# Kernel optimization log

Measured on AMD Instinct MI355X. Metric: run time of the kernel, lower is better.

## Reference

```python
import jax, jax.numpy as jnp
import numpy as np

ITEM_NUM = 50000
EMBED = 256          # d4 = 64, d2 = 128
HIDDEN = 128
BETA = 0.5
BATCH = 4096
HIST = 50
K_NEAR = 10


def setup_inputs() -> dict:
    key = jax.random.key(0)
    ks = jax.random.split(key, 12)
    d4, d2 = EMBED // 4, EMBED // 2
    return {
        "history": jax.random.randint(ks[0], (BATCH, HIST), 0, ITEM_NUM),
        "target": jax.random.randint(ks[1], (BATCH,), 0, ITEM_NUM),
        "near_pois": jax.random.randint(ks[2], (ITEM_NUM, K_NEAR), 0, ITEM_NUM),
        "target_region": jax.random.randint(ks[3], (BATCH,), 0, 1000),
        "E_in": jax.random.normal(ks[4], (ITEM_NUM, d4), jnp.float32) * 0.01,
        "E_out": jax.random.normal(ks[5], (ITEM_NUM, d4), jnp.float32) * 0.01,
        "E_hist": jax.random.normal(ks[6], (ITEM_NUM, d2), jnp.float32) * 0.01,
        "E_targ": jax.random.normal(ks[7], (ITEM_NUM, d2), jnp.float32) * 0.01,
        "W1": jax.random.normal(ks[8], (HIDDEN, EMBED), jnp.float32) * 0.02,
        "b1": jnp.zeros((HIDDEN,), jnp.float32),
        "W2": jax.random.normal(ks[9], (1, HIDDEN), jnp.float32) * 0.02,
    }


def _self_attn(q_src, kv):
    # q = row 0 of q_src; key is a RESHAPE (not transpose) of kv, faithful to torch code.
    N, K, d = kv.shape
    q = q_src[:, 0:1, :]                      # [N,1,d]
    k = kv.reshape(N, d, K)                   # [N,d,K] (reshape, matching torch)
    scores = jnp.einsum('nod,ndk->nok', q, k) / jnp.sqrt(jnp.float32(d))
    w = jax.nn.softmax(scores, axis=-1)       # [N,1,K]
    return jnp.einsum('nok,nkd->nod', w, kv)[:, 0, :]  # [N,d]


def reference(history, target, near_pois, target_region,
              E_in, E_out, E_hist, E_targ, W1, b1, W2):
    ingoing = E_in[near_pois]                 # [N,K,d4]
    outgoing = E_out[near_pois]               # [N,K,d4]
    region_out = _self_attn(ingoing, outgoing)   # [N,d4]
    region_in = _self_attn(outgoing, ingoing)    # [N,d4]

    hist_region = jnp.concatenate([region_in[history], region_out[history]], -1)  # [B,H,d2]
    targ_region = jnp.concatenate([region_out[target], region_in[target]], -1)    # [B,d2]

    hist = jnp.concatenate([E_hist[history], hist_region], -1)      # [B,H,E]
    targ = jnp.concatenate([E_targ[target], targ_region], -1)       # [B,E]

    x = hist * targ[:, None, :]                                     # [B,H,E]
    h1 = jax.nn.relu(x @ W1.T + b1)                                 # [B,H,hidden] (dropout = eval/identity)
    scores = (h1 @ W2.T)[..., 0]                                    # [B,H]

    mask = (history != target[:, None])
    expA = jnp.exp(scores) * mask                                   # [B,H]
    denom = jnp.sum(expA, axis=-1) ** BETA                          # [B], power-normalized (non-softmax)
    w = expA / denom[:, None]                                       # [B,H]

    pred = jnp.einsum('bhe,bh,be->b', hist, w, targ)                # weighted bmm reduction
    return jax.nn.sigmoid(pred)
```

## Files before the change

### kernel.cpp

```cpp
#include <hip/hip_runtime.h>
#include <hip/hip_bf16.h>
#include <math.h>

#define EMBED 256
#define HIDDEN 128
#define NBATCH 4096
#define HISTN 50
#define KNEAR 10
#define D4 64
#define ITEMN 50000
#define XSB 272

#define SH 64.0f
#define SW 32.0f
#define INV_SXSW (1.0f / 32768.0f)
#define INV_SX (1.0f / 1024.0f)

typedef __attribute__((ext_vector_type(4))) float floatx4;
typedef __attribute__((ext_vector_type(2))) float floatx2;

__device__ inline unsigned short f2bf(float f) {
    union { __hip_bfloat16 h; unsigned short u; } cv;
    cv.h = __float2bfloat16(f);
    return cv.u;
}
__device__ inline float bf2f(unsigned short u) {
    return __uint_as_float(((unsigned)u) << 16);
}
__device__ inline unsigned pack2(float a, float b) {
    return (unsigned)f2bf(a) | ((unsigned)f2bf(b) << 16);
}
__device__ inline unsigned pk_fp8x4(float a, float b, float c, float d) {
    int v = __builtin_amdgcn_cvt_pk_fp8_f32(a, b, 0, false);
    v = __builtin_amdgcn_cvt_pk_fp8_f32(c, d, v, true);
    return (unsigned)v;
}
__device__ inline void up_fp8x4(unsigned u, float* f) {
    floatx2 lo = __builtin_amdgcn_cvt_pk_f32_fp8((int)u, false);
    floatx2 hi = __builtin_amdgcn_cvt_pk_f32_fp8((int)u, true);
    f[0] = lo.x; f[1] = lo.y; f[2] = hi.x; f[3] = hi.y;
}

template<int CTRL>
__device__ __forceinline__ float dppf(float x) {
    return __uint_as_float((unsigned)__builtin_amdgcn_update_dpp(
        0, (int)__float_as_uint(x), CTRL, 0xF, 0xF, true));
}
#define DPP_XOR1 0xB1
#define DPP_XOR2 0x4E
#define DPP_HMIR 0x141
#define DPP_MIR  0x140

__global__ __launch_bounds__(256) void fuse1(
    const int* __restrict__ np,
    const float* __restrict__ E_in, const float* __restrict__ E_out,
    const float* __restrict__ E_hist, const float* __restrict__ W1,
    unsigned char* __restrict__ histT, unsigned char* __restrict__ W1s)
{
    __shared__ unsigned short tb_all[4][20 * 64];

    if (blockIdx.x < ITEMN / 4) {
        const int wv = threadIdx.x >> 6;
        const int lane = threadIdx.x & 63;
        const int n = blockIdx.x * 4 + wv;
        unsigned short* tb = tb_all[wv];

        const int g16 = lane >> 4, c16 = lane & 15;

#pragma unroll
        for (int j = 0; j < 5; ++j) {
            int cr = 4 * j + g16;
            int rsel = (cr < 10) ? cr : cr - 10;
            int item = np[n * KNEAR + rsel];
            const float* srcf = ((cr < 10) ? E_in : E_out)
                                + (size_t)item * D4 + c16 * 4;
            float4 v = *(const float4*)srcf;
            uint2 w;
            w.x = pack2(v.x, v.y);
            w.y = pack2(v.z, v.w);
            *(uint2*)&tb[cr * 64 + c16 * 4] = w;
        }
        __asm__ volatile("s_waitcnt lgkmcnt(0)" ::: "memory");

        const int kk = c16;
        const int par = lane & 1, cp = lane >> 1;

#pragma unroll
        for (int pass = 0; pass < 2; ++pass) {
            const int qb = pass ? 640 : 0;
            const int kb = pass ? 0 : 640;

            uint4 qa = *(const uint4*)&tb[qb + g16 * 16];
            uint4 qc = *(const uint4*)&tb[qb + g16 * 16 + 8];
            float qf[16];
            {
                unsigned wds[8] = {qa.x, qa.y, qa.z, qa.w, qc.x, qc.y, qc.z, qc.w};
#pragma unroll
                for (int m = 0; m < 8; ++m) {
                    qf[2 * m]     = bf2f((unsigned short)(wds[m] & 0xffff));
                    qf[2 * m + 1] = bf2f((unsigned short)(wds[m] >> 16));
                }
            }

            const unsigned short* kvp = &tb[kb + g16 * 160 + kk];
            float p = 0.f;
#pragma unroll
            for (int i = 0; i < 16; ++i)
                p = fmaf(bf2f(kvp[10 * i]), qf[i], p);
            p += __shfl_xor(p, 16);
            p += __shfl_xor(p, 32);
            float sc = p * 0.125f;

            float mv = (kk < 10) ? sc : -1e30f;
            mv = fmaxf(mv, dppf<DPP_XOR1>(mv));
            mv = fmaxf(mv, dppf<DPP_XOR2>(mv));
            mv = fmaxf(mv, dppf<DPP_HMIR>(mv));
            mv = fmaxf(mv, dppf<DPP_MIR>(mv));
            float e = (kk < 10) ? __expf(sc - mv) : 0.f;
            float s = e;
            s += dppf<DPP_XOR1>(s);
            s += dppf<DPP_XOR2>(s);
            s += dppf<DPP_HMIR>(s);
            s += dppf<DPP_MIR>(s);
            float w = e / s;

            float oc0 = 0.f, oc1 = 0.f;
#pragma unroll
            for (int q = 0; q < 5; ++q) {
                float we = __uint_as_float(__builtin_amdgcn_readlane(__float_as_uint(w), 2 * q));
                float wo = __uint_as_float(__builtin_amdgcn_readlane(__float_as_uint(w), 2 * q + 1));
                float ws = par ? wo : we;
                unsigned v = *(const unsigned*)&tb[kb + (2 * q + par) * 64 + cp * 2];
                oc0 = fmaf(bf2f((unsigned short)(v & 0xffff)), ws, oc0);
                oc1 = fmaf(bf2f((unsigned short)(v >> 16)), ws, oc1);
            }
            oc0 += dppf<DPP_XOR1>(oc0);
            oc1 += dppf<DPP_XOR1>(oc1);
            if (!par) {
                unsigned char* dst = histT + (size_t)n * 256
                                     + (pass ? 128 : 192) + cp * 2;
                int v2 = __builtin_amdgcn_cvt_pk_fp8_f32(oc0 * SH, oc1 * SH, 0, false);
                *(unsigned short*)dst = (unsigned short)(v2 & 0xffff);
            }
        }
        return;
    }

    long t = (long)(blockIdx.x - ITEMN / 4) * 256 + threadIdx.x;
    if (t < (long)ITEMN * 16) {
        int row = (int)(t >> 4);
        int c8 = ((int)t & 15) * 8;
        const float4* s = (const float4*)&E_hist[(size_t)row * 128 + c8];
        float4 a = s[0], b = s[1];
        uint2 o;
        o.x = pk_fp8x4(a.x * SH, a.y * SH, a.z * SH, a.w * SH);
        o.y = pk_fp8x4(b.x * SH, b.y * SH, b.z * SH, b.w * SH);
        *(uint2*)&histT[(size_t)row * 256 + c8] = o;
        return;
    }
    t -= (long)ITEMN * 16;
    if (t < 4096) {
        int l = (int)t & 63;
        int f = (int)t >> 6;
        int k = f >> 3, nt = f & 7;
        int row = nt * 16 + (l & 15);
        int col = k * 32 + ((l >> 4) << 3);
        const float* src = W1 + row * EMBED + col;
        uint2 o;
        o.x = pk_fp8x4(src[0] * SW, src[1] * SW, src[2] * SW, src[3] * SW);
        o.y = pk_fp8x4(src[4] * SW, src[5] * SW, src[6] * SW, src[7] * SW);
        *(uint2*)&W1s[(size_t)t * 8] = o;
    }
}

__global__ __launch_bounds__(256, 6) void score_kernel(
    const int* __restrict__ history, const int* __restrict__ target,
    const unsigned char* __restrict__ histT,
    const float* __restrict__ E_targ,
    const unsigned char* __restrict__ W1s,
    const float* __restrict__ b1, const float* __restrict__ W2,
    float* __restrict__ out)
{
    __shared__ __align__(16) unsigned char Xs[64][XSB];
    __shared__ float scoreP[4][64];
    __shared__ float rowsumS[64];

    const int t = threadIdx.x;
    const int lane = t & 63;
    const int wv = t >> 6;
    const int b = blockIdx.x;
    const int ti = target[b];
    const int nt0 = wv * 2;
    const int c4 = lane * 4;

    float tgs[4];
    if (c4 < 128) {
        float4 v = *(const float4*)&E_targ[(size_t)ti * 128 + c4];
        tgs[0] = v.x * 16.f; tgs[1] = v.y * 16.f;
        tgs[2] = v.z * 16.f; tgs[3] = v.w * 16.f;
    } else {
        int src = (c4 < 192) ? (c4 + 64) : (c4 - 64);
        unsigned u = *(const unsigned*)&histT[(size_t)ti * 256 + src];
        float f[4]; up_fp8x4(u, f);
        tgs[0] = f[0] * 0.25f; tgs[1] = f[1] * 0.25f;
        tgs[2] = f[2] * 0.25f; tgs[3] = f[3] * 0.25f;
    }

#pragma unroll 4
    for (int h = wv; h < HISTN; h += 4) {
        int item = history[b * HISTN + h];
        unsigned u = *(const unsigned*)&histT[(size_t)item * 256 + c4];
        float f[4]; up_fp8x4(u, f);
        *(unsigned*)&Xs[h][c4] =
            pk_fp8x4(f[0] * tgs[0], f[1] * tgs[1], f[2] * tgs[2], f[3] * tgs[3]);
    }
    __syncthreads();

    floatx4 acc[4][2];
    floatx4 accr = (floatx4){0.f, 0.f, 0.f, 0.f};
#pragma unroll
    for (int m = 0; m < 4; ++m)
#pragma unroll
        for (int n = 0; n < 2; ++n) acc[m][n] = (floatx4){0.f, 0.f, 0.f, 0.f};

    const int ar = lane & 15;
    const int kb8 = (lane >> 4) << 3;
    const long* W1f = (const long*)W1s;
    const long ones = 0x3838383838383838L;

#pragma unroll
    for (int k = 0; k < 8; ++k) {
        long a0 = *(const long*)&Xs[ar][k * 32 + kb8];
        long a1 = *(const long*)&Xs[16 + ar][k * 32 + kb8];
        long a2 = *(const long*)&Xs[32 + ar][k * 32 + kb8];
        long a3 = *(const long*)&Xs[48 + ar][k * 32 + kb8];
        long ax = *(const long*)&Xs[wv * 16 + ar][k * 32 + kb8];
        long bq0 = W1f[(k * 8 + nt0) * 64 + lane];
        long bq1 = W1f[(k * 8 + nt0 + 1) * 64 + lane];
        acc[0][0] = __builtin_amdgcn_mfma_f32_16x16x32_fp8_fp8(a0, bq0, acc[0][0], 0, 0, 0);
        acc[0][1] = __builtin_amdgcn_mfma_f32_16x16x32_fp8_fp8(a0, bq1, acc[0][1], 0, 0, 0);
        acc[1][0] = __builtin_amdgcn_mfma_f32_16x16x32_fp8_fp8(a1, bq0, acc[1][0], 0, 0, 0);
        acc[1][1] = __builtin_amdgcn_mfma_f32_16x16x32_fp8_fp8(a1, bq1, acc[1][1], 0, 0, 0);
        acc[2][0] = __builtin_amdgcn_mfma_f32_16x16x32_fp8_fp8(a2, bq0, acc[2][0], 0, 0, 0);
        acc[2][1] = __builtin_amdgcn_mfma_f32_16x16x32_fp8_fp8(a2, bq1, acc[2][1], 0, 0, 0);
        acc[3][0] = __builtin_amdgcn_mfma_f32_16x16x32_fp8_fp8(a3, bq0, acc[3][0], 0, 0, 0);
        acc[3][1] = __builtin_amdgcn_mfma_f32_16x16x32_fp8_fp8(a3, bq1, acc[3][1], 0, 0, 0);
        accr      = __builtin_amdgcn_mfma_f32_16x16x32_fp8_fp8(ax, ones, accr, 0, 0, 0);
    }

    if (ar == 0) {
        int hb = wv * 16 + ((lane >> 4) << 2);
        rowsumS[hb + 0] = accr[0] * INV_SX;
        rowsumS[hb + 1] = accr[1] * INV_SX;
        rowsumS[hb + 2] = accr[2] * INV_SX;
        rowsumS[hb + 3] = accr[3] * INV_SX;
    }

    float w2v[2], b1v[2];
#pragma unroll
    for (int n = 0; n < 2; ++n) {
        int o = (nt0 + n) * 16 + ar;
        w2v[n] = W2[o];
        b1v[n] = b1[o];
    }
#pragma unroll
    for (int m = 0; m < 4; ++m) {
        float p[4] = {0.f, 0.f, 0.f, 0.f};
#pragma unroll
        for (int n = 0; n < 2; ++n)
#pragma unroll
            for (int r = 0; r < 4; ++r)
                p[r] += w2v[n] * fmaxf(acc[m][n][r] * INV_SXSW + b1v[n], 0.f);
#pragma unroll
        for (int r = 0; r < 4; ++r) {
            float v = p[r];
            v += __shfl_xor(v, 1); v += __shfl_xor(v, 2);
            v += __shfl_xor(v, 4); v += __shfl_xor(v, 8);
            if (ar == 0) scoreP[wv][m * 16 + ((lane >> 4) << 2) + r] = v;
        }
    }
    __syncthreads();

    if (wv == 0) {
        float e = 0.f, er = 0.f;
        if (lane < HISTN) {
            int item = history[b * HISTN + lane];
            float sc = scoreP[0][lane] + scoreP[1][lane] + scoreP[2][lane] + scoreP[3][lane];
            e = (item != ti) ? expf(sc) : 0.f;
            er = e * rowsumS[lane];
        }
#pragma unroll
        for (int off = 1; off < 64; off <<= 1) {
            e += __shfl_xor(e, off);
            er += __shfl_xor(er, off);
        }
        if (lane == 0) {
            float pred = er / sqrtf(e);
            out[b] = 1.f / (1.f + expf(-pred));
        }
    }
}

extern "C" void kernel_launch(void* const* d_in, const int* in_sizes, int n_in,
                              void* d_out, int out_size, void* d_ws, size_t ws_size,
                              hipStream_t stream) {
    const int* history = (const int*)d_in[0];
    const int* target = (const int*)d_in[1];
    const int* near_pois = (const int*)d_in[2];
    const float* E_in = (const float*)d_in[4];
    const float* E_out = (const float*)d_in[5];
    const float* E_hist = (const float*)d_in[6];
    const float* E_targ = (const float*)d_in[7];
    const float* W1 = (const float*)d_in[8];
    const float* b1 = (const float*)d_in[9];
    const float* W2 = (const float*)d_in[10];
    float* out = (float*)d_out;

    unsigned char* W1s = (unsigned char*)d_ws;
    unsigned char* histT = W1s + 32768;

    const int prepBlocks = (int)(((long)ITEMN * 16 + 4096 + 255) / 256);
    fuse1<<<ITEMN / 4 + prepBlocks, 256, 0, stream>>>(
        near_pois, E_in, E_out, E_hist, W1, histT, W1s);
    score_kernel<<<NBATCH, 256, 0, stream>>>(
        history, target, histT, E_targ, W1s, b1, W2, out);
}
```

Baseline: 74.61 us.

## Pre-pack E_in/E_out rows to interleaved fp16 table and batch history gathers

Adds a prep kernel that converts E_in and E_out into one fp16 table with both embeddings of an item interleaved in a single 256-byte row. The region-attention kernel then gathers one row per neighbour instead of two separate fp32 rows, which halves gather traffic and the number of random accesses, and it uses fp16 in place of bf16 for the intermediate values. The score kernel issues all history gathers up front into registers before the conversion loop to raise memory-level parallelism. The cost is an extra kernel launch, an extra full pass over both tables, and more registers in the score kernel.

```diff
diff --git a/kernel.cpp b/kernel.cpp
--- a/kernel.cpp
+++ b/kernel.cpp
@@ -10,6 +10,7 @@
 #define D4 64
 #define ITEMN 50000
 #define XSB 272
+#define RBLK (ITEMN / 4)
 
 #define SH 64.0f
 #define SW 32.0f
@@ -18,17 +19,16 @@
 
 typedef __attribute__((ext_vector_type(4))) float floatx4;
 typedef __attribute__((ext_vector_type(2))) float floatx2;
-
-__device__ inline unsigned short f2bf(float f) {
-    union { __hip_bfloat16 h; unsigned short u; } cv;
-    cv.h = __float2bfloat16(f);
+typedef __attribute__((ext_vector_type(2))) __fp16 half2v;
+
+__device__ inline unsigned pkh2(float a, float b) {
+    union { half2v h; unsigned u; } cv;
+    cv.h = __builtin_amdgcn_cvt_pkrtz(a, b);
     return cv.u;
 }
-__device__ inline float bf2f(unsigned short u) {
-    return __uint_as_float(((unsigned)u) << 16);
-}
-__device__ inline unsigned pack2(float a, float b) {
-    return (unsigned)f2bf(a) | ((unsigned)f2bf(b) << 16);
+__device__ inline float h2f(unsigned short u) {
+    union { unsigned short u; __fp16 h; } cv; cv.u = u;
+    return (float)cv.h;
 }
 __device__ inline unsigned pk_fp8x4(float a, float b, float c, float d) {
     int v = __builtin_amdgcn_cvt_pk_fp8_f32(a, b, 0, false);
@@ -51,34 +51,45 @@
 #define DPP_HMIR 0x141
 #define DPP_MIR  0x140
 
-__global__ __launch_bounds__(256) void fuse1(
+__global__ __launch_bounds__(256) void prep_eio(
+    const float* __restrict__ E_in, const float* __restrict__ E_out,
+    unsigned short* __restrict__ EioT)
+{
+    int tid = blockIdx.x * 256 + threadIdx.x;
+    int row = tid >> 4, c = tid & 15;
+    const float* src = (c < 8) ? &E_in[(size_t)row * 64 + (c & 7) * 8]
+                               : &E_out[(size_t)row * 64 + (c & 7) * 8];
+    float4 a = ((const float4*)src)[0];
+    float4 b = ((const float4*)src)[1];
+    uint4 o;
+    o.x = pkh2(a.x, a.y); o.y = pkh2(a.z, a.w);
+    o.z = pkh2(b.x, b.y); o.w = pkh2(b.z, b.w);
+    *(uint4*)&EioT[(size_t)row * 128 + c * 8] = o;
+}
+
+__global__ __launch_bounds__(256) void regions3(
     const int* __restrict__ np,
-    const float* __restrict__ E_in, const float* __restrict__ E_out,
+    const unsigned short* __restrict__ EioT,
     const float* __restrict__ E_hist, const float* __restrict__ W1,
     unsigned char* __restrict__ histT, unsigned char* __restrict__ W1s)
 {
-    __shared__ unsigned short tb_all[4][20 * 64];
-
-    if (blockIdx.x < ITEMN / 4) {
+    __shared__ unsigned short tiles[4][2][KNEAR * D4];
+
+    if (blockIdx.x < RBLK) {
         const int wv = threadIdx.x >> 6;
         const int lane = threadIdx.x & 63;
         const int n = blockIdx.x * 4 + wv;
-        unsigned short* tb = tb_all[wv];
-
         const int g16 = lane >> 4, c16 = lane & 15;
-
-#pragma unroll
-        for (int j = 0; j < 5; ++j) {
-            int cr = 4 * j + g16;
-            int rsel = (cr < 10) ? cr : cr - 10;
-            int item = np[n * KNEAR + rsel];
-            const float* srcf = ((cr < 10) ? E_in : E_out)
-                                + (size_t)item * D4 + c16 * 4;
-            float4 v = *(const float4*)srcf;
-            uint2 w;
-            w.x = pack2(v.x, v.y);
-            w.y = pack2(v.z, v.w);
-            *(uint2*)&tb[cr * 64 + c16 * 4] = w;
+        const int half = c16 >> 3, col = (c16 & 7) * 8;
+
+#pragma unroll
+        for (int j = 0; j < 3; ++j) {
+            int r = j * 4 + g16;
+            if (r < KNEAR) {
+                int item = np[n * KNEAR + r];
+                uint4 v = *(const uint4*)&EioT[(size_t)item * 128 + c16 * 8];
+                *(uint4*)&tiles[wv][half][r * 64 + col] = v;
+            }
         }
         __asm__ volatile("s_waitcnt lgkmcnt(0)" ::: "memory");
 
@@ -87,26 +98,26 @@
 
 #pragma unroll
         for (int pass = 0; pass < 2; ++pass) {
-            const int qb = pass ? 640 : 0;
-            const int kb = pass ? 0 : 640;
-
-            uint4 qa = *(const uint4*)&tb[qb + g16 * 16];
-            uint4 qc = *(const uint4*)&tb[qb + g16 * 16 + 8];
+            const unsigned short* qrow = tiles[wv][pass];
+            const unsigned short* kvt = tiles[wv][1 - pass];
+
             float qf[16];
             {
-                unsigned wds[8] = {qa.x, qa.y, qa.z, qa.w, qc.x, qc.y, qc.z, qc.w};
+                uint4 qa = *(const uint4*)&qrow[g16 * 16];
+                uint4 qb = *(const uint4*)&qrow[g16 * 16 + 8];
+                unsigned wd[8] = {qa.x, qa.y, qa.z, qa.w, qb.x, qb.y, qb.z, qb.w};
 #pragma unroll
                 for (int m = 0; m < 8; ++m) {
-                    qf[2 * m]     = bf2f((unsigned short)(wds[m] & 0xffff));
-                    qf[2 * m + 1] = bf2f((unsigned short)(wds[m] >> 16));
+                    qf[2 * m]     = h2f((unsigned short)(wd[m] & 0xffff));
+                    qf[2 * m + 1] = h2f((unsigned short)(wd[m] >> 16));
                 }
             }
 
-            const unsigned short* kvp = &tb[kb + g16 * 160 + kk];
+            const unsigned short* kvp = &kvt[g16 * 160 + kk];
             float p = 0.f;
 #pragma unroll
             for (int i = 0; i < 16; ++i)
-                p = fmaf(bf2f(kvp[10 * i]), qf[i], p);
+                p = fmaf(h2f(kvp[10 * i]), qf[i], p);
             p += __shfl_xor(p, 16);
             p += __shfl_xor(p, 32);
             float sc = p * 0.125f;
@@ -130,9 +141,9 @@
                 float we = __uint_as_float(__builtin_amdgcn_readlane(__float_as_uint(w), 2 * q));
                 float wo = __uint_as_float(__builtin_amdgcn_readlane(__float_as_uint(w), 2 * q + 1));
                 float ws = par ? wo : we;
-                unsigned v = *(const unsigned*)&tb[kb + (2 * q + par) * 64 + cp * 2];
-                oc0 = fmaf(bf2f((unsigned short)(v & 0xffff)), ws, oc0);
-                oc1 = fmaf(bf2f((unsigned short)(v >> 16)), ws, oc1);
+                unsigned v = *(const unsigned*)&kvt[(2 * q + par) * 64 + cp * 2];
+                oc0 = fmaf(h2f((unsigned short)(v & 0xffff)), ws, oc0);
+                oc1 = fmaf(h2f((unsigned short)(v >> 16)), ws, oc1);
             }
             oc0 += dppf<DPP_XOR1>(oc0);
             oc1 += dppf<DPP_XOR1>(oc1);
@@ -146,7 +157,7 @@
         return;
     }
 
-    long t = (long)(blockIdx.x - ITEMN / 4) * 256 + threadIdx.x;
+    long t = (long)(blockIdx.x - RBLK) * 256 + threadIdx.x;
     if (t < (long)ITEMN * 16) {
         int row = (int)(t >> 4);
         int c8 = ((int)t & 15) * 8;
@@ -193,6 +204,18 @@
     const int nt0 = wv * 2;
     const int c4 = lane * 4;
 
+    unsigned uu[13];
+    int hrow[13];
+#pragma unroll
+    for (int j = 0; j < 13; ++j) {
+        int h = wv + j * 4;
+        hrow[j] = h;
+        if (h < HISTN) {
+            int item = history[b * HISTN + h];
+            uu[j] = *(const unsigned*)&histT[(size_t)item * 256 + c4];
+        }
+    }
+
     float tgs[4];
     if (c4 < 128) {
         float4 v = *(const float4*)&E_targ[(size_t)ti * 128 + c4];
@@ -206,13 +229,13 @@
         tgs[2] = f[2] * 0.25f; tgs[3] = f[3] * 0.25f;
     }
 
-#pragma unroll 4
-    for (int h = wv; h < HISTN; h += 4) {
-        int item = history[b * HISTN + h];
-        unsigned u = *(const unsigned*)&histT[(size_t)item * 256 + c4];
-        float f[4]; up_fp8x4(u, f);
-        *(unsigned*)&Xs[h][c4] =
-            pk_fp8x4(f[0] * tgs[0], f[1] * tgs[1], f[2] * tgs[2], f[3] * tgs[3]);
+#pragma unroll
+    for (int j = 0; j < 13; ++j) {
+        if (hrow[j] < HISTN) {
+            float f[4]; up_fp8x4(uu[j], f);
+            *(unsigned*)&Xs[hrow[j]][c4] =
+                pk_fp8x4(f[0] * tgs[0], f[1] * tgs[1], f[2] * tgs[2], f[3] * tgs[3]);
+        }
     }
     __syncthreads();
 
@@ -318,10 +341,14 @@
 
     unsigned char* W1s = (unsigned char*)d_ws;
     unsigned char* histT = W1s + 32768;
-
-    const int prepBlocks = (int)(((long)ITEMN * 16 + 4096 + 255) / 256);
-    fuse1<<<ITEMN / 4 + prepBlocks, 256, 0, stream>>>(
-        near_pois, E_in, E_out, E_hist, W1, histT, W1s);
+    unsigned short* EioT = (unsigned short*)(histT + (size_t)ITEMN * 256);
+
+    prep_eio<<<(ITEMN * 16) / 256, 256, 0, stream>>>(E_in, E_out, EioT);
+
+    const int tailBlocks = (int)(((long)ITEMN * 16 + 4096 + 255) / 256);
+    regions3<<<RBLK + tailBlocks, 256, 0, stream>>>(
+        near_pois, EioT, E_hist, W1, histT, W1s);
+
     score_kernel<<<NBATCH, 256, 0, stream>>>(
         history, target, histT, E_targ, W1s, b1, W2, out);
 }
```

New measurement: 69.18 us. 7.3% less time.
